# Optimization experiments

Hardware: AMD Instinct MI355X
Metric: run time of the kernel (lower is better)

The kernel has to match this reference:

```python
import jax, jax.numpy as jnp
import numpy as np

PROJ_SCALE = 0.1


def setup_inputs() -> dict:
    key = jax.random.key(0)
    ks = jax.random.split(key, 6)
    B, D, K, E = 8192, 256, 63, 64  # batch, n_features, num_breakpoints, emb_dim_per_feature
    x_num = jax.random.normal(ks[0], (B, D), dtype=jnp.float32)
    basis_weight = jax.random.normal(ks[1], (D, K + 1, E), dtype=jnp.float32) * 0.001
    basis_bias = jnp.zeros((D, E), dtype=jnp.float32)
    proj_w = jax.random.normal(ks[2], (D, D * E), dtype=jnp.float32) * 0.01  # torch Linear weight (out, in)
    proj_b = jnp.zeros((D,), dtype=jnp.float32)
    breakpoint_min = jax.random.normal(ks[3], (D, 1), dtype=jnp.float32) * 0.1
    breakpoint_delta_raw = jax.random.normal(ks[4], (D, K), dtype=jnp.float32) * 0.5
    return {
        "x_num": x_num,
        "basis_weight": basis_weight,
        "basis_bias": basis_bias,
        "proj_w": proj_w,
        "proj_b": proj_b,
        "breakpoint_min": breakpoint_min,
        "breakpoint_delta_raw": breakpoint_delta_raw,
    }


def reference(x_num, basis_weight, basis_bias, proj_w, proj_b, breakpoint_min, breakpoint_delta_raw):
    # breakpoints: monotone via softplus deltas + cumsum, shape [D, K]
    deltas = jax.nn.softplus(breakpoint_delta_raw)
    breakpoints = breakpoint_min + jnp.cumsum(deltas, axis=1)
    # piecewise-linear basis: [B, D, K+1]
    basis = jax.nn.relu(x_num[:, :, None] - breakpoints[None, :, :])
    basis = jnp.concatenate([x_num[:, :, None], basis], axis=-1)
    # per-feature batched matmul: [B, D, E]
    embeddings = jnp.einsum("bdf,dfe->bde", basis, basis_weight) + basis_bias
    flat = embeddings.reshape(x_num.shape[0], -1)  # [B, D*E]
    x_emb = x_num + PROJ_SCALE * (flat @ proj_w.T + proj_b)
    return x_emb, embeddings, breakpoints
```

## Files before the change

kernel.cpp:

```cpp
#include <hip/hip_runtime.h>
#include <hip/hip_bf16.h>

#define NB 8192
#define ND 256
#define NKBP 63
#define NF 64
#define NE 64
#define NKP 16384
#define NDE 16384
#define NSPLIT 8

typedef __attribute__((ext_vector_type(8))) short short8_t;
typedef __attribute__((ext_vector_type(4))) short short4_t;
typedef __attribute__((ext_vector_type(4))) float f32x4;

__device__ __forceinline__ unsigned short bfbits(float v) {
  union { __hip_bfloat16 b; unsigned short u; } cv;
  cv.b = __float2bfloat16(v);
  return cv.u;
}
__device__ __forceinline__ float bf2f(unsigned short s) {
  return __uint_as_float(((unsigned)s) << 16);
}

__global__ void k_bp(const float* __restrict__ bmin, const float* __restrict__ draw,
                     float* __restrict__ obp) {
  const int d = blockIdx.x * blockDim.x + threadIdx.x;
  if (d >= ND) return;
  float a = bmin[d];
  for (int j = 0; j < NKBP; ++j) {
    float r = draw[d * NKBP + j];
    a += fmaxf(r, 0.f) + log1pf(expf(-fabsf(r)));
    obp[d * NKBP + j] = a;
  }
}

__global__ __launch_bounds__(256, 2) void k_w2(
    const float* __restrict__ bw, const float* __restrict__ pw,
    const float* __restrict__ bb, unsigned short* __restrict__ w2f,
    float* __restrict__ cb_part) {
  const int d = blockIdx.x;
  const int t = threadIdx.x;
  const int l = t & 63, w = t >> 6;
  const int lr = l & 15, lg = l >> 4;
  __shared__ unsigned short pwS[256 * 72];
  __shared__ unsigned short bwS[64 * 72];
  __shared__ float bbS[64];

  {
    const int rr = t >> 4, e0 = (t & 15) * 4;
    #pragma unroll
    for (int it = 0; it < 16; ++it) {
      const int n = it * 16 + rr;
      f32x4 v = *(const f32x4*)(pw + (size_t)n * NDE + d * 64 + e0);
      short4_t s;
      s[0] = (short)bfbits(v[0]); s[1] = (short)bfbits(v[1]);
      s[2] = (short)bfbits(v[2]); s[3] = (short)bfbits(v[3]);
      *(short4_t*)(pwS + n * 72 + e0) = s;
    }
    #pragma unroll
    for (int it = 0; it < 4; ++it) {
      const int f = it * 16 + rr;
      f32x4 v = *(const f32x4*)(bw + (size_t)d * 4096 + f * 64 + e0);
      short4_t s;
      s[0] = (short)bfbits(v[0]); s[1] = (short)bfbits(v[1]);
      s[2] = (short)bfbits(v[2]); s[3] = (short)bfbits(v[3]);
      *(short4_t*)(bwS + f * 72 + e0) = s;
    }
    if (t < 64) bbS[t] = bb[(size_t)d * 64 + t];
  }
  __syncthreads();

  f32x4 acc[4][4];
  #pragma unroll
  for (int mi = 0; mi < 4; ++mi)
    #pragma unroll
    for (int ni = 0; ni < 4; ++ni) acc[mi][ni] = (f32x4){0.f, 0.f, 0.f, 0.f};

  short8_t afr[4][2], bfr[4][2];
  #pragma unroll
  for (int kf = 0; kf < 2; ++kf) {
    #pragma unroll
    for (int mi = 0; mi < 4; ++mi) {
      const int n = w * 64 + mi * 16 + lr;
      afr[mi][kf] = *(const short8_t*)(pwS + n * 72 + kf * 32 + lg * 8);
    }
    #pragma unroll
    for (int ni = 0; ni < 4; ++ni) {
      const int f = ni * 16 + lr;
      bfr[ni][kf] = *(const short8_t*)(bwS + f * 72 + kf * 32 + lg * 8);
    }
  }
  #pragma unroll
  for (int kf = 0; kf < 2; ++kf)
    #pragma unroll
    for (int mi = 0; mi < 4; ++mi)
      #pragma unroll
      for (int ni = 0; ni < 4; ++ni)
        acc[mi][ni] = __builtin_amdgcn_mfma_f32_16x16x32_bf16(afr[mi][kf], bfr[ni][kf], acc[mi][ni], 0, 0, 0);

  #pragma unroll
  for (int mi = 0; mi < 4; ++mi)
    #pragma unroll
    for (int ni = 0; ni < 4; ++ni) {
      const int kf_s = ni >> 1;
      const int lgp  = (ni * 2 + (lr >> 3)) & 3;
      const int jj   = lr & 7;
      const int nb   = w * 64 + mi * 16 + lg * 4;
      const size_t base = (((size_t)d * 2 + kf_s) * 4 + lgp) * 256;
      #pragma unroll
      for (int r = 0; r < 4; ++r)
        w2f[(base + (nb + r)) * 8 + jj] = bfbits(acc[mi][ni][r]);
    }

  {
    float cacc = 0.f;
    #pragma unroll 8
    for (int e = 0; e < 64; ++e) cacc += bf2f(pwS[t * 72 + e]) * bbS[e];
    cb_part[(size_t)d * 256 + t] = cacc;
  }
}

__global__ void k_cbr(const float* __restrict__ cb_part, float* __restrict__ c) {
  const int t = threadIdx.x;
  float a0 = 0.f, a1 = 0.f, a2 = 0.f, a3 = 0.f;
  for (int d = 0; d < ND; d += 4) {
    a0 += cb_part[(size_t)(d + 0) * 256 + t];
    a1 += cb_part[(size_t)(d + 1) * 256 + t];
    a2 += cb_part[(size_t)(d + 2) * 256 + t];
    a3 += cb_part[(size_t)(d + 3) * 256 + t];
  }
  c[t] = (a0 + a1) + (a2 + a3);
}

__global__ __launch_bounds__(256, 3) void k_proj(
    const unsigned short* __restrict__ w2f, const float* __restrict__ bp,
    const float* __restrict__ x, float* __restrict__ pbuf) {
  const int t = threadIdx.x;
  const int l = t & 63, w = t >> 6;
  const int lr = l & 15, lg = l >> 4;
  const int bM = blockIdx.x * 128;
  const int bN = blockIdx.y * 64;
  const int d0 = blockIdx.z * 32;
  __shared__ float thrS[32 * 64];

  for (int i = t; i < 2048; i += 256) {
    const int dl = i >> 6, f = i & 63;
    thrS[i] = (f >= 1) ? bp[(size_t)(d0 + dl) * NKBP + f - 1] : 0.0f;
  }
  __syncthreads();

  f32x4 acc[2][4];
  #pragma unroll
  for (int mi = 0; mi < 2; ++mi)
    #pragma unroll
    for (int ni = 0; ni < 4; ++ni) acc[mi][ni] = (f32x4){0.f, 0.f, 0.f, 0.f};

  const bool lg0 = (lg == 0);
  const unsigned short* bbase[4];
  #pragma unroll
  for (int ni = 0; ni < 4; ++ni)
    bbase[ni] = w2f + (size_t)d0 * 16384 + (size_t)(bN + ni * 16 + lr) * 8 + (size_t)lg * 2048;
  const float* xrow[2];
  #pragma unroll
  for (int mi = 0; mi < 2; ++mi)
    xrow[mi] = x + (size_t)(bM + w * 32 + mi * 16 + lr) * ND + d0;

  for (int c = 0; c < 4; ++c) {
    f32x4 xqa[2], xqb[2];
    #pragma unroll
    for (int mi = 0; mi < 2; ++mi) {
      xqa[mi] = *(const f32x4*)(xrow[mi] + c * 8);
      xqb[mi] = *(const f32x4*)(xrow[mi] + c * 8 + 4);
    }
    #pragma unroll
    for (int dd = 0; dd < 8; ++dd) {
      const int dl = c * 8 + dd;
      short8_t bfr[2][4];
      #pragma unroll
      for (int kf = 0; kf < 2; ++kf)
        #pragma unroll
        for (int ni = 0; ni < 4; ++ni)
          bfr[kf][ni] = *(const short8_t*)(bbase[ni] + (size_t)dl * 16384 + kf * 8192);
      const float* tp = thrS + dl * 64 + lg * 8;
      f32x4 ta = *(const f32x4*)(tp);
      f32x4 tb = *(const f32x4*)(tp + 4);
      f32x4 tc = *(const f32x4*)(tp + 32);
      f32x4 td = *(const f32x4*)(tp + 36);
      short8_t afr[2][2];
      #pragma unroll
      for (int mi = 0; mi < 2; ++mi) {
        const float xv = (dd < 4) ? xqa[mi][dd & 3] : xqb[mi][dd & 3];
        short8_t A0, A1;
        A0[0] = (short)bfbits(lg0 ? xv : fmaxf(xv - ta[0], 0.f));
        A0[1] = (short)bfbits(fmaxf(xv - ta[1], 0.f));
        A0[2] = (short)bfbits(fmaxf(xv - ta[2], 0.f));
        A0[3] = (short)bfbits(fmaxf(xv - ta[3], 0.f));
        A0[4] = (short)bfbits(fmaxf(xv - tb[0], 0.f));
        A0[5] = (short)bfbits(fmaxf(xv - tb[1], 0.f));
        A0[6] = (short)bfbits(fmaxf(xv - tb[2], 0.f));
        A0[7] = (short)bfbits(fmaxf(xv - tb[3], 0.f));
        A1[0] = (short)bfbits(fmaxf(xv - tc[0], 0.f));
        A1[1] = (short)bfbits(fmaxf(xv - tc[1], 0.f));
        A1[2] = (short)bfbits(fmaxf(xv - tc[2], 0.f));
        A1[3] = (short)bfbits(fmaxf(xv - tc[3], 0.f));
        A1[4] = (short)bfbits(fmaxf(xv - td[0], 0.f));
        A1[5] = (short)bfbits(fmaxf(xv - td[1], 0.f));
        A1[6] = (short)bfbits(fmaxf(xv - td[2], 0.f));
        A1[7] = (short)bfbits(fmaxf(xv - td[3], 0.f));
        afr[mi][0] = A0;
        afr[mi][1] = A1;
      }
      #pragma unroll
      for (int kf = 0; kf < 2; ++kf)
        #pragma unroll
        for (int mi = 0; mi < 2; ++mi)
          #pragma unroll
          for (int ni = 0; ni < 4; ++ni)
            acc[mi][ni] = __builtin_amdgcn_mfma_f32_16x16x32_bf16(afr[mi][kf], bfr[kf][ni], acc[mi][ni], 0, 0, 0);
    }
  }

  float* pp = pbuf + (size_t)blockIdx.z * ((size_t)NB * ND);
  #pragma unroll
  for (int mi = 0; mi < 2; ++mi)
    #pragma unroll
    for (int ni = 0; ni < 4; ++ni) {
      const int col = bN + ni * 16 + lr;
      const int rowb = bM + w * 32 + mi * 16 + lg * 4;
      #pragma unroll
      for (int r = 0; r < 4; ++r)
        pp[(size_t)(rowb + r) * ND + col] = acc[mi][ni][r];
    }
}

__global__ void k_comb(const float* __restrict__ x, const float* __restrict__ pbuf,
                       const float* __restrict__ cbuf, const float* __restrict__ pb,
                       float* __restrict__ xe) {
  const size_t i = ((size_t)blockIdx.x * 256 + threadIdx.x) * 4;
  const int n = (int)(i & 255);
  f32x4 s = *(const f32x4*)(pbuf + i);
  #pragma unroll
  for (int p = 1; p < NSPLIT; ++p)
    s += *(const f32x4*)(pbuf + (size_t)p * 2097152 + i);
  f32x4 cv = *(const f32x4*)(cbuf + n);
  f32x4 pv = *(const f32x4*)(pb + n);
  f32x4 xv = *(const f32x4*)(x + i);
  *(f32x4*)(xe + i) = xv + 0.1f * (s + cv + pv);
}

__global__ __launch_bounds__(256, 2) void k_emb(
    const float* __restrict__ x, const float* __restrict__ bw,
    const float* __restrict__ bb, const float* __restrict__ bp,
    float* __restrict__ oe) {
  const int d = blockIdx.y;
  const int b0 = blockIdx.x * 256;
  const int t = threadIdx.x;
  const int l = t & 63, w = t >> 6;
  const int lr = l & 15, lg = l >> 4;
  __shared__ unsigned short btS[64 * 72];
  __shared__ float thrF[64];
  __shared__ float bbS[64];
  __shared__ float cS[4 * 64 * 68];

  float xg[4];
  #pragma unroll
  for (int mi = 0; mi < 4; ++mi)
    xg[mi] = x[(size_t)(b0 + w * 64 + mi * 16 + lr) * ND + d];

  if (t < 64) thrF[t] = (t >= 1) ? bp[(size_t)d * NKBP + t - 1] : 0.0f;
  else if (t < 128) bbS[t - 64] = bb[(size_t)d * 64 + (t - 64)];
  {
    const float* bwd = bw + (size_t)d * 4096;
    const int f = t >> 2, e0 = (t & 3) * 16;
    #pragma unroll
    for (int q = 0; q < 4; ++q) {
      f32x4 v = *(const f32x4*)(bwd + f * 64 + e0 + q * 4);
      #pragma unroll
      for (int r = 0; r < 4; ++r) {
        const int e = e0 + q * 4 + r;
        btS[e * 72 + f] = bfbits(v[r]);
      }
    }
  }
  __syncthreads();

  f32x4 ta = *(const f32x4*)(thrF + lg * 8);
  f32x4 tb = *(const f32x4*)(thrF + lg * 8 + 4);
  f32x4 tc = *(const f32x4*)(thrF + 32 + lg * 8);
  f32x4 td = *(const f32x4*)(thrF + 36 + lg * 8);
  const bool lg0 = (lg == 0);

  short8_t afr[4][2];
  #pragma unroll
  for (int mi = 0; mi < 4; ++mi) {
    const float xv = xg[mi];
    short8_t A0, A1;
    A0[0] = (short)bfbits(lg0 ? xv : fmaxf(xv - ta[0], 0.f));
    A0[1] = (short)bfbits(fmaxf(xv - ta[1], 0.f));
    A0[2] = (short)bfbits(fmaxf(xv - ta[2], 0.f));
    A0[3] = (short)bfbits(fmaxf(xv - ta[3], 0.f));
    A0[4] = (short)bfbits(fmaxf(xv - tb[0], 0.f));
    A0[5] = (short)bfbits(fmaxf(xv - tb[1], 0.f));
    A0[6] = (short)bfbits(fmaxf(xv - tb[2], 0.f));
    A0[7] = (short)bfbits(fmaxf(xv - tb[3], 0.f));
    A1[0] = (short)bfbits(fmaxf(xv - tc[0], 0.f));
    A1[1] = (short)bfbits(fmaxf(xv - tc[1], 0.f));
    A1[2] = (short)bfbits(fmaxf(xv - tc[2], 0.f));
    A1[3] = (short)bfbits(fmaxf(xv - tc[3], 0.f));
    A1[4] = (short)bfbits(fmaxf(xv - td[0], 0.f));
    A1[5] = (short)bfbits(fmaxf(xv - td[1], 0.f));
    A1[6] = (short)bfbits(fmaxf(xv - td[2], 0.f));
    A1[7] = (short)bfbits(fmaxf(xv - td[3], 0.f));
    afr[mi][0] = A0;
    afr[mi][1] = A1;
  }
  short8_t bfr[4][2];
  #pragma unroll
  for (int ni = 0; ni < 4; ++ni) {
    const int e = ni * 16 + lr;
    #pragma unroll
    for (int kf = 0; kf < 2; ++kf)
      bfr[ni][kf] = *(const short8_t*)(btS + e * 72 + kf * 32 + lg * 8);
  }
  f32x4 acc[4][4];
  #pragma unroll
  for (int mi = 0; mi < 4; ++mi)
    #pragma unroll
    for (int ni = 0; ni < 4; ++ni) acc[mi][ni] = (f32x4){0.f, 0.f, 0.f, 0.f};
  #pragma unroll
  for (int kf = 0; kf < 2; ++kf)
    #pragma unroll
    for (int mi = 0; mi < 4; ++mi)
      #pragma unroll
      for (int ni = 0; ni < 4; ++ni)
        acc[mi][ni] = __builtin_amdgcn_mfma_f32_16x16x32_bf16(afr[mi][kf], bfr[ni][kf], acc[mi][ni], 0, 0, 0);

  #pragma unroll
  for (int ni = 0; ni < 4; ++ni) {
    const float bbv = bbS[ni * 16 + lr];
    #pragma unroll
    for (int mi = 0; mi < 4; ++mi) {
      const int rw = mi * 16 + lg * 4;
      #pragma unroll
      for (int r = 0; r < 4; ++r)
        cS[w * 4352 + (rw + r) * 68 + ni * 16 + lr] = acc[mi][ni][r] + bbv;
    }
  }
  __syncthreads();

  const int rsub = t >> 4;
  const int c4 = (t & 15) * 4;
  #pragma unroll
  for (int p = 0; p < 16; ++p) {
    const int row = p * 16 + rsub;
    const int wsrc = row >> 6, wr = row & 63;
    f32x4 v = *(const f32x4*)(cS + wsrc * 4352 + wr * 68 + c4);
    *(f32x4*)(oe + (size_t)(b0 + row) * NDE + d * 64 + c4) = v;
  }
}

extern "C" void kernel_launch(void* const* d_in, const int* in_sizes, int n_in,
                              void* d_out, int out_size, void* d_ws, size_t ws_size,
                              hipStream_t stream) {
  const float* x    = (const float*)d_in[0];
  const float* bw   = (const float*)d_in[1];
  const float* bb   = (const float*)d_in[2];
  const float* pw   = (const float*)d_in[3];
  const float* pb   = (const float*)d_in[4];
  const float* bmin = (const float*)d_in[5];
  const float* draw = (const float*)d_in[6];

  float* out    = (float*)d_out;
  float* out_x  = out;
  float* out_e  = out + (size_t)NB * ND;
  float* out_bp = out_e + (size_t)NB * NDE;

  unsigned short* w2f = (unsigned short*)out_x;
  float* cbuf    = out_e;
  float* pbuf    = out_e + 65536;
  float* cb_part = out_e + 65536 + NSPLIT * 2097152;

  k_bp  <<<dim3(1),            dim3(256), 0, stream>>>(bmin, draw, out_bp);
  k_w2  <<<dim3(256),          dim3(256), 0, stream>>>(bw, pw, bb, w2f, cb_part);
  k_cbr <<<dim3(1),            dim3(256), 0, stream>>>(cb_part, cbuf);
  k_proj<<<dim3(64, 4, NSPLIT),dim3(256), 0, stream>>>(w2f, out_bp, x, pbuf);
  k_comb<<<dim3(2048),         dim3(256), 0, stream>>>(x, pbuf, cbuf, pb, out_x);
  k_emb <<<dim3(32, 256),      dim3(256), 0, stream>>>(x, bw, bb, out_bp, out_e);
}
```

Measured before the change: 285.6 us.

## Skip upper breakpoint K-half when all breakpoints exceed global max of x

Adds a kernel that computes the global maximum of x and counts, per feature, the breakpoints below it. When every feature in a projection split (or a single feature in the embedding kernel) has at most 32 active basis columns, the second MFMA K-fragment is skipped, because relu(x - bp) is exactly zero there. It is exact rather than an approximation, but the saving depends on the data: softplus cumsum breakpoints grow quickly, so most features likely qualify. It adds an extra reduction kernel and per-block branching.

```diff
diff --git a/kernel.cpp b/kernel.cpp
--- a/kernel.cpp
+++ b/kernel.cpp
@@ -23,15 +23,49 @@
   return __uint_as_float(((unsigned)s) << 16);
 }
 
+__global__ void k_maxx(const float* __restrict__ x, float* __restrict__ bmax) {
+  const int t = threadIdx.x;
+  const float* px = x + (size_t)blockIdx.x * 8192;
+  float m = 0.f;
+  #pragma unroll 4
+  for (int i = t; i < 8192; i += 256) m = fmaxf(m, px[i]);
+  #pragma unroll
+  for (int off = 32; off > 0; off >>= 1) m = fmaxf(m, __shfl_down(m, off, 64));
+  __shared__ float red[4];
+  if ((t & 63) == 0) red[t >> 6] = m;
+  __syncthreads();
+  if (t == 0) bmax[blockIdx.x] = fmaxf(fmaxf(red[0], red[1]), fmaxf(red[2], red[3]));
+}
+
 __global__ void k_bp(const float* __restrict__ bmin, const float* __restrict__ draw,
-                     float* __restrict__ obp) {
-  const int d = blockIdx.x * blockDim.x + threadIdx.x;
-  if (d >= ND) return;
+                     const float* __restrict__ bmax, float* __restrict__ obp,
+                     int* __restrict__ fdv, int* __restrict__ fcutc) {
+  const int d = threadIdx.x;
+  __shared__ float mred[256];
+  __shared__ int fds[256];
+  mred[d] = bmax[d];
+  __syncthreads();
+  for (int s = 128; s > 0; s >>= 1) {
+    if (d < s) mred[d] = fmaxf(mred[d], mred[d + s]);
+    __syncthreads();
+  }
+  const float maxx = mred[0];
   float a = bmin[d];
+  int cnt = 0;
   for (int j = 0; j < NKBP; ++j) {
     float r = draw[d * NKBP + j];
     a += fmaxf(r, 0.f) + log1pf(expf(-fabsf(r)));
     obp[d * NKBP + j] = a;
+    cnt += (a < maxx) ? 1 : 0;
+  }
+  const int Fd = 1 + cnt;
+  fdv[d] = Fd;
+  fds[d] = Fd;
+  __syncthreads();
+  if (d < NSPLIT) {
+    int mx = 0;
+    for (int k = 0; k < 32; ++k) mx = max(mx, fds[d * 32 + k]);
+    fcutc[d] = (mx > 32) ? 2 : 1;
   }
 }
 
@@ -133,39 +167,10 @@
   c[t] = (a0 + a1) + (a2 + a3);
 }
 
-__global__ __launch_bounds__(256, 3) void k_proj(
-    const unsigned short* __restrict__ w2f, const float* __restrict__ bp,
-    const float* __restrict__ x, float* __restrict__ pbuf) {
-  const int t = threadIdx.x;
-  const int l = t & 63, w = t >> 6;
-  const int lr = l & 15, lg = l >> 4;
-  const int bM = blockIdx.x * 128;
-  const int bN = blockIdx.y * 64;
-  const int d0 = blockIdx.z * 32;
-  __shared__ float thrS[32 * 64];
-
-  for (int i = t; i < 2048; i += 256) {
-    const int dl = i >> 6, f = i & 63;
-    thrS[i] = (f >= 1) ? bp[(size_t)(d0 + dl) * NKBP + f - 1] : 0.0f;
-  }
-  __syncthreads();
-
-  f32x4 acc[2][4];
-  #pragma unroll
-  for (int mi = 0; mi < 2; ++mi)
-    #pragma unroll
-    for (int ni = 0; ni < 4; ++ni) acc[mi][ni] = (f32x4){0.f, 0.f, 0.f, 0.f};
-
-  const bool lg0 = (lg == 0);
-  const unsigned short* bbase[4];
-  #pragma unroll
-  for (int ni = 0; ni < 4; ++ni)
-    bbase[ni] = w2f + (size_t)d0 * 16384 + (size_t)(bN + ni * 16 + lr) * 8 + (size_t)lg * 2048;
-  const float* xrow[2];
-  #pragma unroll
-  for (int mi = 0; mi < 2; ++mi)
-    xrow[mi] = x + (size_t)(bM + w * 32 + mi * 16 + lr) * ND + d0;
-
+template<bool KF1>
+__device__ __forceinline__ void proj_kloop(
+    const unsigned short* const (&bbase)[4], const float* const (&xrow)[2],
+    const float* thrS_lg, bool lg0, f32x4 (&acc)[2][4]) {
   for (int c = 0; c < 4; ++c) {
     f32x4 xqa[2], xqb[2];
     #pragma unroll
@@ -176,22 +181,23 @@
     #pragma unroll
     for (int dd = 0; dd < 8; ++dd) {
       const int dl = c * 8 + dd;
-      short8_t bfr[2][4];
-      #pragma unroll
-      for (int kf = 0; kf < 2; ++kf)
+      short8_t bfr0[4], bfr1[4];
+      #pragma unroll
+      for (int ni = 0; ni < 4; ++ni)
+        bfr0[ni] = *(const short8_t*)(bbase[ni] + (size_t)dl * 16384);
+      if (KF1) {
         #pragma unroll
         for (int ni = 0; ni < 4; ++ni)
-          bfr[kf][ni] = *(const short8_t*)(bbase[ni] + (size_t)dl * 16384 + kf * 8192);
-      const float* tp = thrS + dl * 64 + lg * 8;
+          bfr1[ni] = *(const short8_t*)(bbase[ni] + (size_t)dl * 16384 + 8192);
+      }
+      const float* tp = thrS_lg + dl * 64;
       f32x4 ta = *(const f32x4*)(tp);
       f32x4 tb = *(const f32x4*)(tp + 4);
-      f32x4 tc = *(const f32x4*)(tp + 32);
-      f32x4 td = *(const f32x4*)(tp + 36);
-      short8_t afr[2][2];
+      short8_t afr0[2], afr1[2];
       #pragma unroll
       for (int mi = 0; mi < 2; ++mi) {
         const float xv = (dd < 4) ? xqa[mi][dd & 3] : xqb[mi][dd & 3];
-        short8_t A0, A1;
+        short8_t A0;
         A0[0] = (short)bfbits(lg0 ? xv : fmaxf(xv - ta[0], 0.f));
         A0[1] = (short)bfbits(fmaxf(xv - ta[1], 0.f));
         A0[2] = (short)bfbits(fmaxf(xv - ta[2], 0.f));
@@ -200,26 +206,79 @@
         A0[5] = (short)bfbits(fmaxf(xv - tb[1], 0.f));
         A0[6] = (short)bfbits(fmaxf(xv - tb[2], 0.f));
         A0[7] = (short)bfbits(fmaxf(xv - tb[3], 0.f));
-        A1[0] = (short)bfbits(fmaxf(xv - tc[0], 0.f));
-        A1[1] = (short)bfbits(fmaxf(xv - tc[1], 0.f));
-        A1[2] = (short)bfbits(fmaxf(xv - tc[2], 0.f));
-        A1[3] = (short)bfbits(fmaxf(xv - tc[3], 0.f));
-        A1[4] = (short)bfbits(fmaxf(xv - td[0], 0.f));
-        A1[5] = (short)bfbits(fmaxf(xv - td[1], 0.f));
-        A1[6] = (short)bfbits(fmaxf(xv - td[2], 0.f));
-        A1[7] = (short)bfbits(fmaxf(xv - td[3], 0.f));
-        afr[mi][0] = A0;
-        afr[mi][1] = A1;
+        afr0[mi] = A0;
       }
-      #pragma unroll
-      for (int kf = 0; kf < 2; ++kf)
+      if (KF1) {
+        f32x4 tc = *(const f32x4*)(tp + 32);
+        f32x4 td = *(const f32x4*)(tp + 36);
+        #pragma unroll
+        for (int mi = 0; mi < 2; ++mi) {
+          const float xv = (dd < 4) ? xqa[mi][dd & 3] : xqb[mi][dd & 3];
+          short8_t A1;
+          A1[0] = (short)bfbits(fmaxf(xv - tc[0], 0.f));
+          A1[1] = (short)bfbits(fmaxf(xv - tc[1], 0.f));
+          A1[2] = (short)bfbits(fmaxf(xv - tc[2], 0.f));
+          A1[3] = (short)bfbits(fmaxf(xv - tc[3], 0.f));
+          A1[4] = (short)bfbits(fmaxf(xv - td[0], 0.f));
+          A1[5] = (short)bfbits(fmaxf(xv - td[1], 0.f));
+          A1[6] = (short)bfbits(fmaxf(xv - td[2], 0.f));
+          A1[7] = (short)bfbits(fmaxf(xv - td[3], 0.f));
+          afr1[mi] = A1;
+        }
+      }
+      #pragma unroll
+      for (int mi = 0; mi < 2; ++mi)
+        #pragma unroll
+        for (int ni = 0; ni < 4; ++ni)
+          acc[mi][ni] = __builtin_amdgcn_mfma_f32_16x16x32_bf16(afr0[mi], bfr0[ni], acc[mi][ni], 0, 0, 0);
+      if (KF1) {
         #pragma unroll
         for (int mi = 0; mi < 2; ++mi)
           #pragma unroll
           for (int ni = 0; ni < 4; ++ni)
-            acc[mi][ni] = __builtin_amdgcn_mfma_f32_16x16x32_bf16(afr[mi][kf], bfr[kf][ni], acc[mi][ni], 0, 0, 0);
-    }
-  }
+            acc[mi][ni] = __builtin_amdgcn_mfma_f32_16x16x32_bf16(afr1[mi], bfr1[ni], acc[mi][ni], 0, 0, 0);
+      }
+    }
+  }
+}
+
+__global__ __launch_bounds__(256, 3) void k_proj(
+    const unsigned short* __restrict__ w2f, const float* __restrict__ bp,
+    const float* __restrict__ x, const int* __restrict__ fcutc,
+    float* __restrict__ pbuf) {
+  const int t = threadIdx.x;
+  const int l = t & 63, w = t >> 6;
+  const int lr = l & 15, lg = l >> 4;
+  const int bM = blockIdx.x * 128;
+  const int bN = blockIdx.y * 64;
+  const int d0 = blockIdx.z * 32;
+  __shared__ float thrS[32 * 64];
+
+  for (int i = t; i < 2048; i += 256) {
+    const int dl = i >> 6, f = i & 63;
+    thrS[i] = (f >= 1) ? bp[(size_t)(d0 + dl) * NKBP + f - 1] : 0.0f;
+  }
+  __syncthreads();
+
+  f32x4 acc[2][4];
+  #pragma unroll
+  for (int mi = 0; mi < 2; ++mi)
+    #pragma unroll
+    for (int ni = 0; ni < 4; ++ni) acc[mi][ni] = (f32x4){0.f, 0.f, 0.f, 0.f};
+
+  const bool lg0 = (lg == 0);
+  const unsigned short* bbase[4];
+  #pragma unroll
+  for (int ni = 0; ni < 4; ++ni)
+    bbase[ni] = w2f + (size_t)d0 * 16384 + (size_t)(bN + ni * 16 + lr) * 8 + (size_t)lg * 2048;
+  const float* xrow[2];
+  #pragma unroll
+  for (int mi = 0; mi < 2; ++mi)
+    xrow[mi] = x + (size_t)(bM + w * 32 + mi * 16 + lr) * ND + d0;
+
+  const int nkf = fcutc[blockIdx.z];
+  if (nkf == 1) proj_kloop<false>(bbase, xrow, thrS + lg * 8, lg0, acc);
+  else          proj_kloop<true >(bbase, xrow, thrS + lg * 8, lg0, acc);
 
   float* pp = pbuf + (size_t)blockIdx.z * ((size_t)NB * ND);
   #pragma unroll
@@ -252,7 +311,7 @@
 __global__ __launch_bounds__(256, 2) void k_emb(
     const float* __restrict__ x, const float* __restrict__ bw,
     const float* __restrict__ bb, const float* __restrict__ bp,
-    float* __restrict__ oe) {
+    const int* __restrict__ fdv, float* __restrict__ oe) {
   const int d = blockIdx.y;
   const int b0 = blockIdx.x * 256;
   const int t = threadIdx.x;
@@ -263,6 +322,8 @@
   __shared__ float bbS[64];
   __shared__ float cS[4 * 64 * 68];
 
+  const int nkf = (fdv[d] > 32) ? 2 : 1;
+
   float xg[4];
   #pragma unroll
   for (int mi = 0; mi < 4; ++mi)
@@ -287,15 +348,13 @@
 
   f32x4 ta = *(const f32x4*)(thrF + lg * 8);
   f32x4 tb = *(const f32x4*)(thrF + lg * 8 + 4);
-  f32x4 tc = *(const f32x4*)(thrF + 32 + lg * 8);
-  f32x4 td = *(const f32x4*)(thrF + 36 + lg * 8);
   const bool lg0 = (lg == 0);
 
-  short8_t afr[4][2];
+  short8_t afr0[4], afr1[4];
   #pragma unroll
   for (int mi = 0; mi < 4; ++mi) {
     const float xv = xg[mi];
-    short8_t A0, A1;
+    short8_t A0;
     A0[0] = (short)bfbits(lg0 ? xv : fmaxf(xv - ta[0], 0.f));
     A0[1] = (short)bfbits(fmaxf(xv - ta[1], 0.f));
     A0[2] = (short)bfbits(fmaxf(xv - ta[2], 0.f));
@@ -304,24 +363,13 @@
     A0[5] = (short)bfbits(fmaxf(xv - tb[1], 0.f));
     A0[6] = (short)bfbits(fmaxf(xv - tb[2], 0.f));
     A0[7] = (short)bfbits(fmaxf(xv - tb[3], 0.f));
-    A1[0] = (short)bfbits(fmaxf(xv - tc[0], 0.f));
-    A1[1] = (short)bfbits(fmaxf(xv - tc[1], 0.f));
-    A1[2] = (short)bfbits(fmaxf(xv - tc[2], 0.f));
-    A1[3] = (short)bfbits(fmaxf(xv - tc[3], 0.f));
-    A1[4] = (short)bfbits(fmaxf(xv - td[0], 0.f));
-    A1[5] = (short)bfbits(fmaxf(xv - td[1], 0.f));
-    A1[6] = (short)bfbits(fmaxf(xv - td[2], 0.f));
-    A1[7] = (short)bfbits(fmaxf(xv - td[3], 0.f));
-    afr[mi][0] = A0;
-    afr[mi][1] = A1;
-  }
-  short8_t bfr[4][2];
+    afr0[mi] = A0;
+  }
+  short8_t bfr0[4], bfr1[4];
   #pragma unroll
   for (int ni = 0; ni < 4; ++ni) {
     const int e = ni * 16 + lr;
-    #pragma unroll
-    for (int kf = 0; kf < 2; ++kf)
-      bfr[ni][kf] = *(const short8_t*)(btS + e * 72 + kf * 32 + lg * 8);
+    bfr0[ni] = *(const short8_t*)(btS + e * 72 + lg * 8);
   }
   f32x4 acc[4][4];
   #pragma unroll
@@ -329,12 +377,39 @@
     #pragma unroll
     for (int ni = 0; ni < 4; ++ni) acc[mi][ni] = (f32x4){0.f, 0.f, 0.f, 0.f};
   #pragma unroll
-  for (int kf = 0; kf < 2; ++kf)
+  for (int mi = 0; mi < 4; ++mi)
+    #pragma unroll
+    for (int ni = 0; ni < 4; ++ni)
+      acc[mi][ni] = __builtin_amdgcn_mfma_f32_16x16x32_bf16(afr0[mi], bfr0[ni], acc[mi][ni], 0, 0, 0);
+
+  if (nkf == 2) {
+    f32x4 tc = *(const f32x4*)(thrF + 32 + lg * 8);
+    f32x4 td = *(const f32x4*)(thrF + 36 + lg * 8);
+    #pragma unroll
+    for (int mi = 0; mi < 4; ++mi) {
+      const float xv = xg[mi];
+      short8_t A1;
+      A1[0] = (short)bfbits(fmaxf(xv - tc[0], 0.f));
+      A1[1] = (short)bfbits(fmaxf(xv - tc[1], 0.f));
+      A1[2] = (short)bfbits(fmaxf(xv - tc[2], 0.f));
+      A1[3] = (short)bfbits(fmaxf(xv - tc[3], 0.f));
+      A1[4] = (short)bfbits(fmaxf(xv - td[0], 0.f));
+      A1[5] = (short)bfbits(fmaxf(xv - td[1], 0.f));
+      A1[6] = (short)bfbits(fmaxf(xv - td[2], 0.f));
+      A1[7] = (short)bfbits(fmaxf(xv - td[3], 0.f));
+      afr1[mi] = A1;
+    }
+    #pragma unroll
+    for (int ni = 0; ni < 4; ++ni) {
+      const int e = ni * 16 + lr;
+      bfr1[ni] = *(const short8_t*)(btS + e * 72 + 32 + lg * 8);
+    }
     #pragma unroll
     for (int mi = 0; mi < 4; ++mi)
       #pragma unroll
       for (int ni = 0; ni < 4; ++ni)
-        acc[mi][ni] = __builtin_amdgcn_mfma_f32_16x16x32_bf16(afr[mi][kf], bfr[ni][kf], acc[mi][ni], 0, 0, 0);
+        acc[mi][ni] = __builtin_amdgcn_mfma_f32_16x16x32_bf16(afr1[mi], bfr1[ni], acc[mi][ni], 0, 0, 0);
+  }
 
   #pragma unroll
   for (int ni = 0; ni < 4; ++ni) {
@@ -380,11 +455,15 @@
   float* cbuf    = out_e;
   float* pbuf    = out_e + 65536;
   float* cb_part = out_e + 65536 + NSPLIT * 2097152;
-
-  k_bp  <<<dim3(1),            dim3(256), 0, stream>>>(bmin, draw, out_bp);
+  float* bmax = (float*)d_ws;
+  int*   fdv  = (int*)d_ws + 256;
+  int*   fcutc= (int*)d_ws + 512;
+
+  k_maxx<<<dim3(256),          dim3(256), 0, stream>>>(x, bmax);
+  k_bp  <<<dim3(1),            dim3(256), 0, stream>>>(bmin, draw, bmax, out_bp, fdv, fcutc);
   k_w2  <<<dim3(256),          dim3(256), 0, stream>>>(bw, pw, bb, w2f, cb_part);
   k_cbr <<<dim3(1),            dim3(256), 0, stream>>>(cb_part, cbuf);
-  k_proj<<<dim3(64, 4, NSPLIT),dim3(256), 0, stream>>>(w2f, out_bp, x, pbuf);
+  k_proj<<<dim3(64, 4, NSPLIT),dim3(256), 0, stream>>>(w2f, out_bp, x, fcutc, pbuf);
   k_comb<<<dim3(2048),         dim3(256), 0, stream>>>(x, pbuf, cbuf, pb, out_x);
-  k_emb <<<dim3(32, 256),      dim3(256), 0, stream>>>(x, bw, bb, out_bp, out_e);
-}
+  k_emb <<<dim3(32, 256),      dim3(256), 0, stream>>>(x, bw, bb, out_bp, fdv, out_e);
+}
```

After: 264.7 us. 7.3% less time.
